# Kernel optimization log

Hardware: AMD Instinct MI355X
Metric: run time of the kernel (lower is better)

## Reference

```python
import jax, jax.numpy as jnp
import numpy as np

B, T, V, E, H = 128, 512, 32000, 256, 128


def _lstm(xw, U, b, reverse):
    """Run an LSTM over time.
    xw: [T, B, 4H] precomputed input projections; U: [H, 4H]; b: [4H].
    Returns (hs [T,B,H], h_T [B,H], c_T [B,H]). Keras gate order i,f,g,o.
    """
    Hd = U.shape[0]
    Bd = xw.shape[1]

    def step(carry, xw_t):
        h, c = carry
        z = xw_t + h @ U + b  # [B, 4H]
        i, f, g, o = jnp.split(z, 4, axis=-1)
        i = jax.nn.sigmoid(i)
        f = jax.nn.sigmoid(f)
        g = jnp.tanh(g)
        o = jax.nn.sigmoid(o)
        c = f * c + i * g
        h = o * jnp.tanh(c)
        return (h, c), h

    h0 = jnp.zeros((Bd, Hd), xw.dtype)
    (hT, cT), hs = jax.lax.scan(step, (h0, h0), xw, reverse=reverse)
    return hs, hT, cT


def setup_inputs() -> dict:
    key = jax.random.key(0)
    ks = jax.random.split(key, 8)
    tokens = jax.random.randint(ks[0], (B, T), 0, V, dtype=jnp.int64)
    emb = jax.random.uniform(ks[1], (V, E), jnp.float32, -0.05, 0.05)
    s_in = 1.0 / np.sqrt(E)
    s_rec = 1.0 / np.sqrt(H)
    W_fw = jax.random.normal(ks[2], (E, 4 * H), jnp.float32) * s_in
    U_fw = jax.random.normal(ks[3], (H, 4 * H), jnp.float32) * s_rec
    b_fw = jnp.zeros((4 * H,), jnp.float32).at[H:2 * H].set(1.0)  # unit forget bias
    W_bw = jax.random.normal(ks[4], (E, 4 * H), jnp.float32) * s_in
    U_bw = jax.random.normal(ks[5], (H, 4 * H), jnp.float32) * s_rec
    b_bw = jnp.zeros((4 * H,), jnp.float32).at[H:2 * H].set(1.0)
    return {"tokens": tokens, "emb": emb,
            "W_fw": W_fw, "U_fw": U_fw, "b_fw": b_fw,
            "W_bw": W_bw, "U_bw": U_bw, "b_bw": b_bw}


def reference(tokens, emb, W_fw, U_fw, b_fw, W_bw, U_bw, b_bw):
    # Embedding lookup (dropout layers are identity at inference)
    x = emb[tokens]                    # [B, T, E]
    xt = jnp.swapaxes(x, 0, 1)         # [T, B, E] time-major for scan
    # Precompute input projections as one big GEMM per direction
    hs_fw, h_fw, c_fw = _lstm(xt @ W_fw, U_fw, b_fw, reverse=False)
    hs_bw, h_bw, c_bw = _lstm(xt @ W_bw, U_bw, b_bw, reverse=True)
    out = jnp.concatenate([hs_fw, hs_bw], axis=-1)  # [T, B, 2H]
    out = jnp.swapaxes(out, 0, 1)                    # [B, T, 2H]
    return out, (h_fw, c_fw), (h_bw, c_bw)
```

## Files before the change

kernel.cpp:

```cpp
#include <hip/hip_runtime.h>
#include <hip/hip_bf16.h>


typedef short short8 __attribute__((ext_vector_type(8)));
typedef float f32x4 __attribute__((ext_vector_type(4)));

#define GLL16(g, l)                                                        \
  __builtin_amdgcn_global_load_lds(                                        \
      (const __attribute__((address_space(1))) void*)(g),                  \
      (__attribute__((address_space(3))) void*)(l), 16, 0, 0)

__device__ __forceinline__ unsigned short f2bf(float f) {
  __hip_bfloat16 h = __float2bfloat16(f);
  return __builtin_bit_cast(unsigned short, h);
}

__device__ __forceinline__ float fast_sigmoid(float z) {
  return 1.f / (1.f + __expf(-z));
}
__device__ __forceinline__ float fast_tanh(float z) {
  return 1.f - 2.f / (__expf(2.f * z) + 1.f);
}

__global__ void prep_emb(const float4* __restrict__ in,
                         ushort4* __restrict__ outp, int n4) {
  int i = blockIdx.x * blockDim.x + threadIdx.x;
  if (i < n4) {
    float4 v = in[i];
    ushort4 o;
    o.x = f2bf(v.x); o.y = f2bf(v.y); o.z = f2bf(v.z); o.w = f2bf(v.w);
    outp[i] = o;
  }
}

__global__ void prep_wt(const float* __restrict__ Wfw,
                        const float* __restrict__ Wbw,
                        __hip_bfloat16* __restrict__ Wt) {
  int n = blockIdx.x;
  int k = threadIdx.x;
  const float* W = (n < 512) ? Wfw : Wbw;
  Wt[n * 256 + k] = __float2bfloat16(W[k * 512 + (n & 511)]);
}

__global__ __launch_bounds__(256) void gemm_xw(
    const int* __restrict__ tokens, const __hip_bfloat16* __restrict__ embb,
    const __hip_bfloat16* __restrict__ Wt, __hip_bfloat16* __restrict__ xw) {
  __shared__ __attribute__((aligned(16))) __hip_bfloat16 As[128 * 32];
  __shared__ __attribute__((aligned(16))) __hip_bfloat16 Bs[128 * 32];
  const int tid = threadIdx.x;
  const int bm = blockIdx.x;
  const int bn = blockIdx.y;
  const int lane = tid & 63, w = tid >> 6;

  const int ar = tid >> 2;
  const int kcol = (tid & 3) * 8;
  const long r0 = (long)bm * 128 + ar;
  const int tok0 = tokens[r0];
  const int tok1 = tokens[r0 + 64];
  const __hip_bfloat16* a0 = embb + (size_t)tok0 * 256 + kcol;
  const __hip_bfloat16* a1 = embb + (size_t)tok1 * 256 + kcol;
  const __hip_bfloat16* bs0 = Wt + ((size_t)bn * 128 + ar) * 256 + kcol;
  const __hip_bfloat16* bs1 = bs0 + 64 * 256;
  __hip_bfloat16* As_d0 = As + tid * 8;
  __hip_bfloat16* As_d1 = As + 2048 + tid * 8;
  __hip_bfloat16* Bs_d0 = Bs + tid * 8;
  __hip_bfloat16* Bs_d1 = Bs + 2048 + tid * 8;

  f32x4 acc[4][4];
#pragma unroll
  for (int i = 0; i < 4; ++i)
#pragma unroll
    for (int j = 0; j < 4; ++j) acc[i][j] = (f32x4){0.f, 0.f, 0.f, 0.f};

  const int fm = (w >> 1) * 64, fn = (w & 1) * 64;
  const int lr = lane & 15, lk = (lane >> 4) * 8;

  for (int kk = 0; kk < 8; ++kk) {
    GLL16(a0 + kk * 32, As_d0);
    GLL16(a1 + kk * 32, As_d1);
    GLL16(bs0 + kk * 32, Bs_d0);
    GLL16(bs1 + kk * 32, Bs_d1);
    __syncthreads();
    short8 af[4], bfr[4];
#pragma unroll
    for (int i = 0; i < 4; ++i)
      af[i] = *(const short8*)(As + (fm + 16 * i + lr) * 32 + lk);
#pragma unroll
    for (int j = 0; j < 4; ++j)
      bfr[j] = *(const short8*)(Bs + (fn + 16 * j + lr) * 32 + lk);
#pragma unroll
    for (int i = 0; i < 4; ++i)
#pragma unroll
      for (int j = 0; j < 4; ++j)
        acc[i][j] = __builtin_amdgcn_mfma_f32_16x16x32_bf16(af[i], bfr[j],
                                                            acc[i][j], 0, 0, 0);
    __syncthreads();
  }

  const int orow = (lane >> 4) * 4;
#pragma unroll
  for (int i = 0; i < 4; ++i)
#pragma unroll
    for (int j = 0; j < 4; ++j)
#pragma unroll
      for (int r = 0; r < 4; ++r) {
        int row_local = fm + 16 * i + orow + r;
        int col_local = fn + 16 * j + (lane & 15);
        size_t rg = (size_t)bm * 128 + row_local;
        int ng = bn * 128 + col_local;
        size_t addr = (size_t)(ng >> 9) * 33554432ull + rg * 512 + (ng & 511);
        xw[addr] = __float2bfloat16(acc[i][j][r]);
      }
}

__global__ void prep_ut(const float* __restrict__ Ufw,
                        const float* __restrict__ Ubw,
                        float* __restrict__ Ut) {
  int idx = blockIdx.x * 512 + threadIdx.x;
  int j = idx & 3;
  int dc = (idx >> 2) & 1023;
  int k4 = idx >> 12;
  int k = 4 * k4 + j;
  int c = dc & 511;
  const float* U = (dc >> 9) ? Ubw : Ufw;
  Ut[idx] = U[k * 512 + c];
}

__global__ __launch_bounds__(512, 1) void lstm_rec(
    const float* __restrict__ Ut, const float* __restrict__ b_fw,
    const float* __restrict__ b_bw, const __hip_bfloat16* __restrict__ xw,
    float* __restrict__ out) {
  __shared__ __attribute__((aligned(16))) float h_lds[128];
  __shared__ float g_lds[512];
  const int tid = threadIdx.x;
  const int dir = blockIdx.x >> 7;
  const int b = blockIdx.x & 127;
  const float bias = (dir ? b_bw : b_fw)[tid];

  f32x4 Uc4[32];
#pragma unroll
  for (int k4 = 0; k4 < 32; ++k4)
    Uc4[k4] = *(const f32x4*)(Ut + ((size_t)k4 * 1024 + dir * 512 + tid) * 4);

  if (tid < 128) h_lds[tid] = 0.f;
  float c = 0.f, h = 0.f, hfin = 0.f;
  __syncthreads();

  const __hip_bfloat16* xb =
      xw + (size_t)dir * 33554432ull + (size_t)b * 262144ull + tid;
  float* outb = out + (size_t)b * 512 * 256 + dir * 128;

  int t = dir ? 511 : 0;
  const int st = dir ? -1 : 1;
  __hip_bfloat16 xc = xb[(size_t)t * 512];
  const float4* h4 = (const float4*)h_lds;
  const int grp = tid >> 7;

  for (int it = 0; it < 512; ++it) {
    const int tn = (it == 511) ? t : (t + st);
    __hip_bfloat16 xn = xb[(size_t)tn * 512];
    float a0 = 0.f, a1 = 0.f, a2 = 0.f, a3 = 0.f;
#pragma unroll
    for (int k4 = 0; k4 < 32; ++k4) {
      float4 hv = h4[k4];
      f32x4 u = Uc4[k4];
      a0 = fmaf(hv.x, u.x, a0);
      a1 = fmaf(hv.y, u.y, a1);
      a2 = fmaf(hv.z, u.z, a2);
      a3 = fmaf(hv.w, u.w, a3);
    }
    float z = __bfloat162float(xc) + bias + ((a0 + a1) + (a2 + a3));
    float act = (grp == 2) ? fast_tanh(z) : fast_sigmoid(z);
    g_lds[tid] = act;
    __syncthreads();
    if (tid < 128) {
      c = g_lds[128 + tid] * c + g_lds[tid] * g_lds[256 + tid];
      h = g_lds[384 + tid] * fast_tanh(c);
      hfin = h;
      h_lds[tid] = h;
    }
    __syncthreads();
    if (tid < 128) outb[(size_t)t * 256 + tid] = h;
    xc = xn;
    t = tn;
  }
  if (tid < 128) {
    float* o2 = out + 16777216;
    o2[dir * 32768 + b * 128 + tid] = hfin;
    o2[dir * 32768 + 16384 + b * 128 + tid] = c;
  }
}

extern "C" void kernel_launch(void* const* d_in, const int* in_sizes, int n_in,
                              void* d_out, int out_size, void* d_ws,
                              size_t ws_size, hipStream_t stream) {
  const int* tokens = (const int*)d_in[0];
  const float* emb = (const float*)d_in[1];
  const float* W_fw = (const float*)d_in[2];
  const float* U_fw = (const float*)d_in[3];
  const float* b_fw = (const float*)d_in[4];
  const float* W_bw = (const float*)d_in[5];
  const float* U_bw = (const float*)d_in[6];
  const float* b_bw = (const float*)d_in[7];
  float* out = (float*)d_out;

  char* ws = (char*)d_ws;
  __hip_bfloat16* embb = (__hip_bfloat16*)(ws);
  __hip_bfloat16* Wt = (__hip_bfloat16*)(ws + 16384000);
  __hip_bfloat16* xw = (__hip_bfloat16*)(ws + 16908288);
  float* Ut = (float*)(ws);

  prep_emb<<<8000, 256, 0, stream>>>((const float4*)emb, (ushort4*)embb,
                                     2048000);
  prep_wt<<<1024, 256, 0, stream>>>(W_fw, W_bw, Wt);
  gemm_xw<<<dim3(512, 8), 256, 0, stream>>>(tokens, embb, Wt, xw);
  prep_ut<<<256, 512, 0, stream>>>(U_fw, U_bw, Ut);
  lstm_rec<<<256, 512, 0, stream>>>(Ut, b_fw, b_bw, xw, out);
}
```

Before: 641.5 us.

## Split LSTM recurrent dot product over two K halves with 1024-thread blocks

The recurrent kernel now uses 1024 threads per block. Each gate column is computed by two threads, each covering half of the hidden dimension, and the partial sums are combined through shared memory. This halves the serial FMA chain per step and the register footprint for U, which should shorten each latency-bound timestep. The cost is one extra shared-memory round trip and barrier per step, plus larger blocks.

```diff
diff --git a/kernel.cpp b/kernel.cpp
--- a/kernel.cpp
+++ b/kernel.cpp
@@ -126,52 +126,69 @@
   Ut[idx] = U[k * 512 + c];
 }
 
-__global__ __launch_bounds__(512, 1) void lstm_rec(
+__global__ __launch_bounds__(1024) void lstm_rec(
     const float* __restrict__ Ut, const float* __restrict__ b_fw,
     const float* __restrict__ b_bw, const __hip_bfloat16* __restrict__ xw,
     float* __restrict__ out) {
   __shared__ __attribute__((aligned(16))) float h_lds[128];
+  __shared__ float pz[1024];
   __shared__ float g_lds[512];
   const int tid = threadIdx.x;
+  const int col = tid & 511;
+  const int kh = tid >> 9;
   const int dir = blockIdx.x >> 7;
   const int b = blockIdx.x & 127;
-  const float bias = (dir ? b_bw : b_fw)[tid];
-
-  f32x4 Uc4[32];
-#pragma unroll
-  for (int k4 = 0; k4 < 32; ++k4)
-    Uc4[k4] = *(const f32x4*)(Ut + ((size_t)k4 * 1024 + dir * 512 + tid) * 4);
+
+  const float* up = Ut + ((size_t)kh * 16 * 1024 + dir * 512 + col) * 4;
+#define ULOAD(j) f32x4 u##j = *(const f32x4*)(up + (j) * 4096);
+  ULOAD(0) ULOAD(1) ULOAD(2) ULOAD(3) ULOAD(4) ULOAD(5) ULOAD(6) ULOAD(7)
+  ULOAD(8) ULOAD(9) ULOAD(10) ULOAD(11) ULOAD(12) ULOAD(13) ULOAD(14) ULOAD(15)
+#undef ULOAD
+  asm volatile("" ::"v"(u0), "v"(u1), "v"(u2), "v"(u3), "v"(u4), "v"(u5),
+               "v"(u6), "v"(u7), "v"(u8), "v"(u9), "v"(u10), "v"(u11),
+               "v"(u12), "v"(u13), "v"(u14), "v"(u15));
 
   if (tid < 128) h_lds[tid] = 0.f;
   float c = 0.f, h = 0.f, hfin = 0.f;
   __syncthreads();
 
+  const float bias = (dir ? b_bw : b_fw)[col];
   const __hip_bfloat16* xb =
-      xw + (size_t)dir * 33554432ull + (size_t)b * 262144ull + tid;
-  float* outb = out + (size_t)b * 512 * 256 + dir * 128;
+      xw + (size_t)dir * 33554432ull + (size_t)b * 262144ull + col;
+  float* outb = out + (size_t)b * 131072 + dir * 128;
 
   int t = dir ? 511 : 0;
   const int st = dir ? -1 : 1;
-  __hip_bfloat16 xc = xb[(size_t)t * 512];
+  __hip_bfloat16 xc = __float2bfloat16(0.f);
+  if (kh) xc = xb[(size_t)t * 512];
   const float4* h4 = (const float4*)h_lds;
-  const int grp = tid >> 7;
+  const int grp = col >> 7;
+  const int hb = kh * 16;
 
   for (int it = 0; it < 512; ++it) {
     const int tn = (it == 511) ? t : (t + st);
-    __hip_bfloat16 xn = xb[(size_t)tn * 512];
+    __hip_bfloat16 xn = xc;
+    if (kh) xn = xb[(size_t)tn * 512];
     float a0 = 0.f, a1 = 0.f, a2 = 0.f, a3 = 0.f;
-#pragma unroll
-    for (int k4 = 0; k4 < 32; ++k4) {
-      float4 hv = h4[k4];
-      f32x4 u = Uc4[k4];
-      a0 = fmaf(hv.x, u.x, a0);
-      a1 = fmaf(hv.y, u.y, a1);
-      a2 = fmaf(hv.z, u.z, a2);
-      a3 = fmaf(hv.w, u.w, a3);
+#define UFMA(j)                                         \
+  {                                                     \
+    float4 hv = h4[hb + (j)];   \
+    a0 = fmaf(hv.x, u##j.x, a0);                        \
+    a1 = fmaf(hv.y, u##j.y, a1);                        \
+    a2 = fmaf(hv.z, u##j.z, a2);                        \
+    a3 = fmaf(hv.w, u##j.w, a3);                        \
+  }
+    UFMA(0) UFMA(1) UFMA(2) UFMA(3) UFMA(4) UFMA(5) UFMA(6) UFMA(7)
+    UFMA(8) UFMA(9) UFMA(10) UFMA(11) UFMA(12) UFMA(13) UFMA(14) UFMA(15)
+#undef UFMA
+    float partial = (a0 + a1) + (a2 + a3);
+    if (kh) partial += __bfloat162float(xc) + bias;
+    pz[tid] = partial;
+    __syncthreads();
+    if (tid < 512) {
+      float z = pz[col] + pz[col + 512];
+      g_lds[col] = (grp == 2) ? fast_tanh(z) : fast_sigmoid(z);
     }
-    float z = __bfloat162float(xc) + bias + ((a0 + a1) + (a2 + a3));
-    float act = (grp == 2) ? fast_tanh(z) : fast_sigmoid(z);
-    g_lds[tid] = act;
     __syncthreads();
     if (tid < 128) {
       c = g_lds[128 + tid] * c + g_lds[tid] * g_lds[256 + tid];
@@ -215,5 +232,5 @@
   prep_wt<<<1024, 256, 0, stream>>>(W_fw, W_bw, Wt);
   gemm_xw<<<dim3(512, 8), 256, 0, stream>>>(tokens, embb, Wt, xw);
   prep_ut<<<256, 512, 0, stream>>>(U_fw, U_bw, Ut);
-  lstm_rec<<<256, 512, 0, stream>>>(Ut, b_fw, b_bw, xw, out);
-}
+  lstm_rec<<<256, 1024, 0, stream>>>(Ut, b_fw, b_bw, xw, out);
+}
```

Result: slower. 735.9 us (+14.7%).
